# Kernel tuning notes

Hardware: AMD Instinct MI355X
Metric: run time of the kernel (lower is better)

The kernel has to match this reference:

```python
import jax, jax.numpy as jnp
import numpy as np

SEQ, D_IN, D_OUT = 8192, 768, 64


def setup_inputs() -> dict:
    key = jax.random.key(0)
    kx, kq, kk, kv = jax.random.split(key, 4)
    scale = 1.0 / np.sqrt(D_IN)
    return {
        "x": jax.random.normal(kx, (SEQ, D_IN), dtype=jnp.float32),
        # torch Linear weight layout: [d_out, d_in]
        "W_Q": jax.random.uniform(kq, (D_OUT, D_IN), dtype=jnp.float32, minval=-scale, maxval=scale),
        "W_K": jax.random.uniform(kk, (D_OUT, D_IN), dtype=jnp.float32, minval=-scale, maxval=scale),
        "W_V": jax.random.uniform(kv, (D_OUT, D_IN), dtype=jnp.float32, minval=-scale, maxval=scale),
    }


def reference(x, W_Q, W_K, W_V):
    # q,k,v: [seq, d_out]
    q = x @ W_Q.T
    k = x @ W_K.T
    v = x @ W_V.T
    scores = (q @ k.T) / jnp.sqrt(jnp.asarray(k.shape[-1], x.dtype))  # [seq, seq]
    attn = jax.nn.softmax(scores, axis=-1)
    return attn @ v  # [seq, d_out]
```

## Files before the change

kernel.cpp:

```cpp
#include <hip/hip_runtime.h>
#include <hip/hip_bf16.h>
#include <math.h>

#define SEQ 8192
#define DIN 768
#define DOUT 64
#define QSCALE 0.1803368801111214f

typedef __attribute__((ext_vector_type(8))) short short8;
typedef __attribute__((ext_vector_type(4))) short short4v;
typedef __attribute__((ext_vector_type(4))) float floatx4;
typedef __attribute__((ext_vector_type(2))) unsigned int uint2v;

__device__ __forceinline__ void gload16(const void* g, void* l) {
    __builtin_amdgcn_global_load_lds(
        (const __attribute__((address_space(1))) unsigned int*)g,
        (__attribute__((address_space(3))) unsigned int*)l, 16, 0, 0);
}

__device__ __forceinline__ unsigned pack2(float a, float b) {
    __hip_bfloat162 h = __float22bfloat162_rn(make_float2(a, b));
    return *(unsigned*)&h;
}

__device__ __forceinline__ unsigned short bfbits(float f) {
    __hip_bfloat16 h = __float2bfloat16(f);
    return *(unsigned short*)&h;
}

__device__ __forceinline__ float exp2r(float x) {
#if __has_builtin(__builtin_amdgcn_exp2f)
    return __builtin_amdgcn_exp2f(x);
#else
    float r; asm("v_exp_f32 %0, %1" : "=v"(r) : "v"(x)); return r;
#endif
}

__device__ __forceinline__ floatx4 max4(floatx4 a, floatx4 b) {
    floatx4 r;
    r[0] = fmaxf(a[0], b[0]); r[1] = fmaxf(a[1], b[1]);
    r[2] = fmaxf(a[2], b[2]); r[3] = fmaxf(a[3], b[3]);
    return r;
}

__device__ __forceinline__ floatx4 mfma16(short4v a, short4v b, floatx4 c) {
#if __has_builtin(__builtin_amdgcn_mfma_f32_16x16x16bf16_1k)
    return __builtin_amdgcn_mfma_f32_16x16x16bf16_1k(a, b, c, 0, 0, 0);
#else
    asm("v_mfma_f32_16x16x16_bf16 %0, %1, %2, %0" : "+v"(c) : "v"(a), "v"(b));
    return c;
#endif
}

__device__ __forceinline__ int phs(int s, int R) {
    return (s & 8) | ((s ^ R) & 7);
}

__global__ __launch_bounds__(256) void prep_w(
    const float* __restrict__ Wq, const float* __restrict__ Wk,
    const float* __restrict__ Wv, unsigned short* __restrict__ wbf)
{
    const int i = blockIdx.x * 256 + threadIdx.x;
    const int base = i * 8;
    const int row = base / DIN;
    const int k = base % DIN;
    const float* src = (row < 64)  ? &Wq[(size_t)row * DIN + k]
                     : (row < 128) ? &Wk[(size_t)(row - 64) * DIN + k]
                                   : &Wv[(size_t)(row - 128) * DIN + k];
    const float4 f0 = *(const float4*)src;
    const float4 f1 = *(const float4*)(src + 4);
    uint4 v;
    v.x = pack2(f0.x, f0.y);
    v.y = pack2(f0.z, f0.w);
    v.z = pack2(f1.x, f1.y);
    v.w = pack2(f1.z, f1.w);
    *(uint4*)&wbf[base] = v;
}

__global__ __launch_bounds__(256) void qkv_mfma(
    const float* __restrict__ x, const unsigned short* __restrict__ wbf,
    unsigned short* __restrict__ qbf, unsigned short* __restrict__ kbf,
    unsigned short* __restrict__ vtbf)
{
    __shared__ __align__(16) unsigned char xs[2][32 * 256];
    __shared__ __align__(16) unsigned char wsm[2][192 * 256];

    const int t = threadIdx.x;
    const int l = t & 63;
    const int wid = t >> 6;
    const int h = wid & 1;
    const int ntb = (wid >> 1) * 6;
    const int q4_ = l & 15;
    const int row0 = blockIdx.x * 32;

    const int Rx_st = t >> 3;
    const int s0    = (t & 7) * 2;
    const int Rr4   = l >> 4;
    const int s16   = l & 15;

    floatx4 acc[6];
#pragma unroll
    for (int i = 0; i < 6; ++i) acc[i] = (floatx4){0.f, 0.f, 0.f, 0.f};

#define STAGE_X(buf, k0)                                                      \
    {                                                                         \
        _Pragma("unroll")                                                     \
        for (int ss = 0; ss < 2; ++ss) {                                      \
            const int sl = s0 + ss;                                           \
            const float4 a = *(const float4*)&x[(size_t)(row0 + Rx_st) * DIN + (k0) + sl * 8]; \
            const float4 b = *(const float4*)&x[(size_t)(row0 + Rx_st) * DIN + (k0) + sl * 8 + 4]; \
            uint4 v;                                                          \
            v.x = pack2(a.x, a.y); v.y = pack2(a.z, a.w);                     \
            v.z = pack2(b.x, b.y); v.w = pack2(b.z, b.w);                     \
            *(uint4*)&xs[buf][Rx_st * 256 + phs(sl, Rx_st) * 16] = v;         \
        }                                                                     \
    }

#define STAGE_W(buf, k0)                                                      \
    {                                                                         \
        _Pragma("unroll")                                                     \
        for (int ss = 0; ss < 12; ++ss) {                                     \
            const int s = wid * 12 + ss;                           \
            const int Rw = 4 * s + Rr4;                           \
            const int slog = (s16 & 8) | ((s16 ^ Rw) & 7);                    \
            gload16(&wbf[(size_t)Rw * DIN + (k0) + slog * 8], &wsm[buf][s * 1024]); \
        }                                                                     \
    }

    STAGE_X(0, 0)
    STAGE_W(0, 0)

    int cur = 0;
    for (int kc = 0; kc < 6; ++kc) {
        __syncthreads();

        float4 xa[2], xb[2];
        const bool more = (kc + 1 < 6);
        if (more) {
            const int k1 = (kc + 1) * 128;
            STAGE_W(cur ^ 1, k1)
#pragma unroll
            for (int ss = 0; ss < 2; ++ss) {
                const int sl = s0 + ss;
                xa[ss] = *(const float4*)&x[(size_t)(row0 + Rx_st) * DIN + k1 + sl * 8];
                xb[ss] = *(const float4*)&x[(size_t)(row0 + Rx_st) * DIN + k1 + sl * 8 + 4];
            }
        }

#pragma unroll
        for (int ks = 0; ks < 4; ++ks) {
            const int g = l >> 4;
            const int slot = g + 4 * ks;
            const int Rxx = h * 16 + q4_;
            const short8 a = *(const short8*)&xs[cur][Rxx * 256 + phs(slot, Rxx) * 16];
#pragma unroll
            for (int j = 0; j < 6; ++j) {
                const int Rw = (ntb + j) * 16 + q4_;
                const short8 b = *(const short8*)&wsm[cur][Rw * 256 + phs(slot, Rw) * 16];
                acc[j] = __builtin_amdgcn_mfma_f32_16x16x32_bf16(a, b, acc[j], 0, 0, 0);
            }
        }

        if (more) {
#pragma unroll
            for (int ss = 0; ss < 2; ++ss) {
                const int sl = s0 + ss;
                uint4 v;
                v.x = pack2(xa[ss].x, xa[ss].y); v.y = pack2(xa[ss].z, xa[ss].w);
                v.z = pack2(xb[ss].x, xb[ss].y); v.w = pack2(xb[ss].z, xb[ss].w);
                *(uint4*)&xs[cur ^ 1][Rx_st * 256 + phs(sl, Rx_st) * 16] = v;
            }
        }
        cur ^= 1;
    }

    const int rb = row0 + h * 16 + ((l >> 4) << 2);
#pragma unroll
    for (int j = 0; j < 6; ++j) {
        const int nt = ntb + j;
#pragma unroll
        for (int r = 0; r < 4; ++r) {
            const float v = acc[j][r];
            const int R = rb + r;
            if (nt < 4) {
                qbf[(size_t)R * 64 + nt * 16 + q4_] = bfbits(v * QSCALE);
            } else if (nt < 8) {
                kbf[(size_t)R * 64 + (nt - 4) * 16 + q4_] = bfbits(v);
            } else {
                vtbf[(size_t)((nt - 8) * 16 + q4_) * SEQ + R] = bfbits(v);
            }
        }
    }
#undef STAGE_X
#undef STAGE_W
}

__global__ __launch_bounds__(256, 4) void flash_mfma(
    const unsigned short* __restrict__ qbf,
    const unsigned short* __restrict__ kbf,
    const unsigned short* __restrict__ vtbf,
    float* __restrict__ opart,
    float* __restrict__ ml,
    int nsplit, int direct)
{
    __shared__ __align__(16) unsigned char lds[32768];
    unsigned char* lkb = lds;
    unsigned char* lvb = lds + 16384;

    const int t = threadIdx.x;
    const int l = t & 63;
    const int g = l >> 4;
    const int q4 = l & 15;
    const int wid = t >> 6;
    const int row0 = blockIdx.x * 64;
    const int split = blockIdx.y;
    const int chunk = SEQ / nsplit;
    const int kbeg = split * chunk;
    const int NT = chunk / 64;

    short8 qf[2];
#pragma unroll
    for (int ks = 0; ks < 2; ++ks)
        qf[ks] = *(const short8*)&qbf[(size_t)(row0 + wid * 16 + q4) * 64 + (g + 4 * ks) * 8];

    {
        const int Rr = l >> 3;
        const int sl = (l & 7) ^ Rr;
#pragma unroll
        for (int ss = 0; ss < 2; ++ss) {
            const int s = wid * 2 + ss;
            const int R = 8 * s + Rr;
            gload16(&kbf[(size_t)(kbeg + R) * 64 + sl * 8], lkb + s * 1024);
            gload16(&vtbf[(size_t)R * SEQ + kbeg + sl * 8], lvb + s * 1024);
        }
    }
    __syncthreads();

    floatx4 oacc[4];
#pragma unroll
    for (int i = 0; i < 4; ++i) oacc[i] = (floatx4){0.f, 0.f, 0.f, 0.f};
    floatx4 l_acc = (floatx4){0.f, 0.f, 0.f, 0.f};
    float m_run = -INFINITY;

    int cur = 0;
    for (int tt = 0; tt < NT; ++tt) {
        const unsigned char* lk = lkb + cur * 8192;
        const unsigned char* lv = lvb + cur * 8192;

        if (tt + 1 < NT) {
            const int kt1 = kbeg + (tt + 1) * 64;
            const int Rr = l >> 3;
            const int sl = (l & 7) ^ Rr;
#pragma unroll
            for (int ss = 0; ss < 2; ++ss) {
                const int s = wid * 2 + ss;
                const int R = 8 * s + Rr;
                gload16(&kbf[(size_t)(kt1 + R) * 64 + sl * 8],
                        lkb + (cur ^ 1) * 8192 + s * 1024);
                gload16(&vtbf[(size_t)R * SEQ + kt1 + sl * 8],
                        lvb + (cur ^ 1) * 8192 + s * 1024);
            }
        }

        floatx4 sacc[4];
#pragma unroll
        for (int i = 0; i < 4; ++i) sacc[i] = (floatx4){0.f, 0.f, 0.f, 0.f};
#pragma unroll
        for (int ks = 0; ks < 2; ++ks) {
            const int sl = g + 4 * ks;
#pragma unroll
            for (int nt = 0; nt < 4; ++nt) {
                const int R = nt * 16 + q4;
                const short8 kf = *(const short8*)&lk[R * 128 + ((sl ^ (R & 7)) << 4)];
                sacc[nt] = __builtin_amdgcn_mfma_f32_16x16x32_bf16(kf, qf[ks], sacc[nt], 0, 0, 0);
            }
        }

        const floatx4 mm = max4(max4(sacc[0], sacc[1]), max4(sacc[2], sacc[3]));
        const float own = fmaxf(fmaxf(mm[0], mm[1]), fmaxf(mm[2], mm[3]));

        if (__any(own > m_run + 8.0f)) {
            float pm = own;
            pm = fmaxf(pm, __shfl_xor(pm, 16));
            pm = fmaxf(pm, __shfl_xor(pm, 32));
            const float mn = fmaxf(m_run, pm);
            const float alpha = exp2r(m_run - mn);
            m_run = mn;
            l_acc *= alpha;
#pragma unroll
            for (int dt = 0; dt < 4; ++dt) oacc[dt] *= alpha;
        }

        floatx4 pv4[4];
#pragma unroll
        for (int nt = 0; nt < 4; ++nt) {
            floatx4 d = sacc[nt];
            d[0] -= m_run; d[1] -= m_run; d[2] -= m_run; d[3] -= m_run;
            pv4[nt][0] = exp2r(d[0]); pv4[nt][1] = exp2r(d[1]);
            pv4[nt][2] = exp2r(d[2]); pv4[nt][3] = exp2r(d[3]);
        }
        l_acc += (pv4[0] + pv4[1]) + (pv4[2] + pv4[3]);

#pragma unroll
        for (int kb = 0; kb < 4; ++kb) {
            const unsigned p0 = pack2(pv4[kb][0], pv4[kb][1]);
            const unsigned p1 = pack2(pv4[kb][2], pv4[kb][3]);
            const short4v bfr = __builtin_bit_cast(short4v, (uint2v){p0, p1});
            const int sl = kb * 2 + (g >> 1);
#pragma unroll
            for (int dt = 0; dt < 4; ++dt) {
                const int R = dt * 16 + q4;
                const short4v a = *(const short4v*)&lv[R * 128 +
                    ((sl ^ (R & 7)) << 4) + ((g & 1) << 3)];
                oacc[dt] = mfma16(a, bfr, oacc[dt]);
            }
        }

        __syncthreads();
        cur ^= 1;
    }

    float l_run = (l_acc[0] + l_acc[1]) + (l_acc[2] + l_acc[3]);
    l_run += __shfl_xor(l_run, 16);
    l_run += __shfl_xor(l_run, 32);

    float* trans = (float*)lds;
    {
        const int qrow = wid * 16 + q4;
        const float sc = direct ? (1.0f / l_run) : 1.0f;
#pragma unroll
        for (int dt = 0; dt < 4; ++dt) {
            floatx4 v = oacc[dt] * sc;
            *(floatx4*)&trans[qrow * 68 + dt * 16 + g * 4] = v;
        }
        if (!direct && l < 16) {
            const size_t mrow = (size_t)split * SEQ + row0 + wid * 16 + l;
            ml[mrow * 2 + 0] = m_run;
            ml[mrow * 2 + 1] = l_run;
        }
    }
    __syncthreads();

    float* outbase = direct ? opart : opart + (size_t)split * SEQ * 64;
#pragma unroll
    for (int it = 0; it < 4; ++it) {
        const int row = it * 16 + (t >> 4);
        const floatx4 v = *(const floatx4*)&trans[row * 68 + (t & 15) * 4];
        *(floatx4*)&outbase[(size_t)(row0 + row) * 64 + (t & 15) * 4] = v;
    }
}

__global__ __launch_bounds__(256) void combine_kernel(
    const float* __restrict__ opart, const float* __restrict__ ml,
    float* __restrict__ out, int nsplit)
{
    const int i4 = blockIdx.x * 256 + threadIdx.x;
    if (i4 >= SEQ * DOUT / 4) return;
    const int row = (i4 * 4) >> 6;

    float M = -INFINITY;
    for (int s = 0; s < nsplit; ++s)
        M = fmaxf(M, ml[((size_t)s * SEQ + row) * 2]);

    float denom = 0.f;
    floatx4 acc = (floatx4){0.f, 0.f, 0.f, 0.f};
    for (int s = 0; s < nsplit; ++s) {
        const float w = exp2r(ml[((size_t)s * SEQ + row) * 2] - M);
        denom += ml[((size_t)s * SEQ + row) * 2 + 1] * w;
        const floatx4 v = *(const floatx4*)&opart[(size_t)s * SEQ * DOUT + i4 * 4];
        acc += v * w;
    }
    acc *= (1.0f / denom);
    *(floatx4*)&out[i4 * 4] = acc;
}

extern "C" void kernel_launch(void* const* d_in, const int* in_sizes, int n_in,
                              void* d_out, int out_size, void* d_ws, size_t ws_size,
                              hipStream_t stream)
{
    const float* x  = (const float*)d_in[0];
    const float* Wq = (const float*)d_in[1];
    const float* Wk = (const float*)d_in[2];
    const float* Wv = (const float*)d_in[3];
    float* out = (float*)d_out;
    unsigned char* ws = (unsigned char*)d_ws;

    const size_t wbf_b = (size_t)192 * DIN * 2;
    const size_t qkv_b = (size_t)SEQ * 64 * 2;
    size_t off = 0;
    unsigned short* wbf  = (unsigned short*)(ws + off); off += wbf_b;
    unsigned short* qbf  = (unsigned short*)(ws + off); off += qkv_b;
    unsigned short* kbf  = (unsigned short*)(ws + off); off += qkv_b;
    unsigned short* vtbf = (unsigned short*)(ws + off); off += qkv_b;

    const size_t per_split = (size_t)SEQ * 64 * 4 + (size_t)SEQ * 2 * 4;
    int nsplit = 0;
    if      (ws_size >= off + 8 * per_split) nsplit = 8;
    else if (ws_size >= off + 4 * per_split) nsplit = 4;
    else if (ws_size >= off + 2 * per_split) nsplit = 2;

    prep_w<<<72, 256, 0, stream>>>(Wq, Wk, Wv, wbf);
    qkv_mfma<<<SEQ / 32, 256, 0, stream>>>(x, wbf, qbf, kbf, vtbf);

    if (nsplit == 0) {
        flash_mfma<<<dim3(SEQ / 64, 1), 256, 0, stream>>>(
            qbf, kbf, vtbf, out, nullptr, 1, 1);
    } else {
        float* opart = (float*)(ws + off);
        float* mlp   = (float*)(ws + off + (size_t)nsplit * SEQ * 64 * 4);
        flash_mfma<<<dim3(SEQ / 64, nsplit), 256, 0, stream>>>(
            qbf, kbf, vtbf, opart, mlp, nsplit, 0);
        combine_kernel<<<(SEQ * DOUT / 4 + 255) / 256, 256, 0, stream>>>(
            opart, mlp, out, nsplit);
    }
}
```

Before: 61.22 us.

## Split key tiles across waves and load K/V straight into registers

The flash kernel is reorganized so each wave owns 16 keys of every 64-key tile for all 64 query rows, instead of owning 16 query rows. K and V fragments are loaded directly from global memory into registers with register prefetch. This removes the LDS double-buffering and the per-iteration block barrier. Partial outputs, maxima and sums from the four waves are merged through LDS at the end. In exchange the kernel needs many more accumulator registers (64 output floats per lane), drops the occupancy hint in launch bounds, and uses a running max shared across query tiles, which could hurt occupancy and numerical range.

```diff
diff --git a/kernel.cpp b/kernel.cpp
--- a/kernel.cpp
+++ b/kernel.cpp
@@ -120,8 +120,8 @@
     {                                                                         \
         _Pragma("unroll")                                                     \
         for (int ss = 0; ss < 12; ++ss) {                                     \
-            const int s = wid * 12 + ss;                           \
-            const int Rw = 4 * s + Rr4;                           \
+            const int s = wid * 12 + ss;                                      \
+            const int Rw = 4 * s + Rr4;                                       \
             const int slog = (s16 & 8) | ((s16 ^ Rw) & 7);                    \
             gload16(&wbf[(size_t)Rw * DIN + (k0) + slog * 8], &wsm[buf][s * 1024]); \
         }                                                                     \
@@ -195,7 +195,7 @@
 #undef STAGE_W
 }
 
-__global__ __launch_bounds__(256, 4) void flash_mfma(
+__global__ __launch_bounds__(256) void flash_mfma(
     const unsigned short* __restrict__ qbf,
     const unsigned short* __restrict__ kbf,
     const unsigned short* __restrict__ vtbf,
@@ -203,14 +203,14 @@
     float* __restrict__ ml,
     int nsplit, int direct)
 {
-    __shared__ __align__(16) unsigned char lds[32768];
-    unsigned char* lkb = lds;
-    unsigned char* lvb = lds + 16384;
+    __shared__ __align__(16) float obuf[2][64 * 68];
+    __shared__ float lbuf[4][64];
+    __shared__ float mbuf[4][16];
 
     const int t = threadIdx.x;
     const int l = t & 63;
+    const int x = l & 15;
     const int g = l >> 4;
-    const int q4 = l & 15;
     const int wid = t >> 6;
     const int row0 = blockIdx.x * 64;
     const int split = blockIdx.y;
@@ -218,62 +218,45 @@
     const int kbeg = split * chunk;
     const int NT = chunk / 64;
 
-    short8 qf[2];
-#pragma unroll
-    for (int ks = 0; ks < 2; ++ks)
-        qf[ks] = *(const short8*)&qbf[(size_t)(row0 + wid * 16 + q4) * 64 + (g + 4 * ks) * 8];
-
-    {
-        const int Rr = l >> 3;
-        const int sl = (l & 7) ^ Rr;
-#pragma unroll
-        for (int ss = 0; ss < 2; ++ss) {
-            const int s = wid * 2 + ss;
-            const int R = 8 * s + Rr;
-            gload16(&kbf[(size_t)(kbeg + R) * 64 + sl * 8], lkb + s * 1024);
-            gload16(&vtbf[(size_t)R * SEQ + kbeg + sl * 8], lvb + s * 1024);
-        }
-    }
-    __syncthreads();
-
-    floatx4 oacc[4];
-#pragma unroll
-    for (int i = 0; i < 4; ++i) oacc[i] = (floatx4){0.f, 0.f, 0.f, 0.f};
-    floatx4 l_acc = (floatx4){0.f, 0.f, 0.f, 0.f};
+    short8 qf[4][2];
+#pragma unroll
+    for (int qt = 0; qt < 4; ++qt)
+#pragma unroll
+        for (int ks = 0; ks < 2; ++ks)
+            qf[qt][ks] = *(const short8*)&qbf[(size_t)(row0 + qt * 16 + x) * 64 + ks * 32 + g * 8];
+
+    const unsigned short* kbase = kbf + (size_t)(kbeg + wid * 16 + x) * 64 + g * 8;
+    const unsigned short* vbase = vtbf + (size_t)x * SEQ + kbeg + wid * 16 + g * 4;
+
+    floatx4 oacc[4][4];
+#pragma unroll
+    for (int i = 0; i < 4; ++i)
+#pragma unroll
+        for (int j = 0; j < 4; ++j) oacc[i][j] = (floatx4){0.f, 0.f, 0.f, 0.f};
+    float l_acc[4] = {0.f, 0.f, 0.f, 0.f};
     float m_run = -INFINITY;
 
-    int cur = 0;
+    short8 kn0 = *(const short8*)(kbase);
+    short8 kn1 = *(const short8*)(kbase + 32);
+
     for (int tt = 0; tt < NT; ++tt) {
-        const unsigned char* lk = lkb + cur * 8192;
-        const unsigned char* lv = lvb + cur * 8192;
-
+        const short8 kc0 = kn0, kc1 = kn1;
         if (tt + 1 < NT) {
-            const int kt1 = kbeg + (tt + 1) * 64;
-            const int Rr = l >> 3;
-            const int sl = (l & 7) ^ Rr;
-#pragma unroll
-            for (int ss = 0; ss < 2; ++ss) {
-                const int s = wid * 2 + ss;
-                const int R = 8 * s + Rr;
-                gload16(&kbf[(size_t)(kt1 + R) * 64 + sl * 8],
-                        lkb + (cur ^ 1) * 8192 + s * 1024);
-                gload16(&vtbf[(size_t)R * SEQ + kt1 + sl * 8],
-                        lvb + (cur ^ 1) * 8192 + s * 1024);
-            }
-        }
+            kn0 = *(const short8*)(kbase + (size_t)(tt + 1) * 4096);
+            kn1 = *(const short8*)(kbase + (size_t)(tt + 1) * 4096 + 32);
+        }
+        short4v vf[4];
+#pragma unroll
+        for (int dt = 0; dt < 4; ++dt)
+            vf[dt] = *(const short4v*)(vbase + (size_t)dt * 16 * SEQ + tt * 64);
 
         floatx4 sacc[4];
 #pragma unroll
         for (int i = 0; i < 4; ++i) sacc[i] = (floatx4){0.f, 0.f, 0.f, 0.f};
 #pragma unroll
-        for (int ks = 0; ks < 2; ++ks) {
-            const int sl = g + 4 * ks;
-#pragma unroll
-            for (int nt = 0; nt < 4; ++nt) {
-                const int R = nt * 16 + q4;
-                const short8 kf = *(const short8*)&lk[R * 128 + ((sl ^ (R & 7)) << 4)];
-                sacc[nt] = __builtin_amdgcn_mfma_f32_16x16x32_bf16(kf, qf[ks], sacc[nt], 0, 0, 0);
-            }
+        for (int qt = 0; qt < 4; ++qt) {
+            sacc[qt] = __builtin_amdgcn_mfma_f32_16x16x32_bf16(kc0, qf[qt][0], sacc[qt], 0, 0, 0);
+            sacc[qt] = __builtin_amdgcn_mfma_f32_16x16x32_bf16(kc1, qf[qt][1], sacc[qt], 0, 0, 0);
         }
 
         const floatx4 mm = max4(max4(sacc[0], sacc[1]), max4(sacc[2], sacc[3]));
@@ -284,69 +267,103 @@
             pm = fmaxf(pm, __shfl_xor(pm, 16));
             pm = fmaxf(pm, __shfl_xor(pm, 32));
             const float mn = fmaxf(m_run, pm);
-            const float alpha = exp2r(m_run - mn);
+            const float al = exp2r(m_run - mn);
             m_run = mn;
-            l_acc *= alpha;
-#pragma unroll
-            for (int dt = 0; dt < 4; ++dt) oacc[dt] *= alpha;
-        }
-
-        floatx4 pv4[4];
-#pragma unroll
-        for (int nt = 0; nt < 4; ++nt) {
-            floatx4 d = sacc[nt];
+#pragma unroll
+            for (int qt = 0; qt < 4; ++qt) {
+                l_acc[qt] *= al;
+#pragma unroll
+                for (int dt = 0; dt < 4; ++dt) oacc[qt][dt] *= al;
+            }
+        }
+
+#pragma unroll
+        for (int qt = 0; qt < 4; ++qt) {
+            floatx4 d = sacc[qt];
             d[0] -= m_run; d[1] -= m_run; d[2] -= m_run; d[3] -= m_run;
-            pv4[nt][0] = exp2r(d[0]); pv4[nt][1] = exp2r(d[1]);
-            pv4[nt][2] = exp2r(d[2]); pv4[nt][3] = exp2r(d[3]);
-        }
-        l_acc += (pv4[0] + pv4[1]) + (pv4[2] + pv4[3]);
-
-#pragma unroll
-        for (int kb = 0; kb < 4; ++kb) {
-            const unsigned p0 = pack2(pv4[kb][0], pv4[kb][1]);
-            const unsigned p1 = pack2(pv4[kb][2], pv4[kb][3]);
-            const short4v bfr = __builtin_bit_cast(short4v, (uint2v){p0, p1});
-            const int sl = kb * 2 + (g >> 1);
+            floatx4 p;
+            p[0] = exp2r(d[0]); p[1] = exp2r(d[1]);
+            p[2] = exp2r(d[2]); p[3] = exp2r(d[3]);
+            l_acc[qt] += (p[0] + p[1]) + (p[2] + p[3]);
+            const unsigned p0 = pack2(p[0], p[1]);
+            const unsigned p1 = pack2(p[2], p[3]);
+            const short4v pb = __builtin_bit_cast(short4v, (uint2v){p0, p1});
+#pragma unroll
+            for (int dt = 0; dt < 4; ++dt)
+                oacc[qt][dt] = mfma16(vf[dt], pb, oacc[qt][dt]);
+        }
+    }
+
+    if (l < 16) mbuf[wid][x] = m_run;
+    __syncthreads();
+
+    const float Mx = fmaxf(fmaxf(mbuf[0][x], mbuf[1][x]),
+                           fmaxf(mbuf[2][x], mbuf[3][x]));
+    const float scale = exp2r(m_run - Mx);
+
+    float lq[4];
+#pragma unroll
+    for (int qt = 0; qt < 4; ++qt) {
+        float s = l_acc[qt];
+        s += __shfl_xor(s, 16);
+        s += __shfl_xor(s, 32);
+        lq[qt] = s * scale;
+    }
+    if (l < 16) {
+#pragma unroll
+        for (int qt = 0; qt < 4; ++qt) lbuf[wid][qt * 16 + x] = lq[qt];
+    }
+
+    float* mybuf = obuf[wid >> 1];
+    if (wid & 1) {
+#pragma unroll
+        for (int qt = 0; qt < 4; ++qt)
+#pragma unroll
+            for (int dt = 0; dt < 4; ++dt)
+                *(floatx4*)&mybuf[(qt * 16 + x) * 68 + dt * 16 + g * 4] =
+                    oacc[qt][dt] * scale;
+    }
+    __syncthreads();
+    if (!(wid & 1)) {
+#pragma unroll
+        for (int qt = 0; qt < 4; ++qt)
 #pragma unroll
             for (int dt = 0; dt < 4; ++dt) {
-                const int R = dt * 16 + q4;
-                const short4v a = *(const short4v*)&lv[R * 128 +
-                    ((sl ^ (R & 7)) << 4) + ((g & 1) << 3)];
-                oacc[dt] = mfma16(a, bfr, oacc[dt]);
-            }
-        }
-
-        __syncthreads();
-        cur ^= 1;
-    }
-
-    float l_run = (l_acc[0] + l_acc[1]) + (l_acc[2] + l_acc[3]);
-    l_run += __shfl_xor(l_run, 16);
-    l_run += __shfl_xor(l_run, 32);
-
-    float* trans = (float*)lds;
-    {
-        const int qrow = wid * 16 + q4;
-        const float sc = direct ? (1.0f / l_run) : 1.0f;
-#pragma unroll
-        for (int dt = 0; dt < 4; ++dt) {
-            floatx4 v = oacc[dt] * sc;
-            *(floatx4*)&trans[qrow * 68 + dt * 16 + g * 4] = v;
-        }
-        if (!direct && l < 16) {
-            const size_t mrow = (size_t)split * SEQ + row0 + wid * 16 + l;
-            ml[mrow * 2 + 0] = m_run;
-            ml[mrow * 2 + 1] = l_run;
-        }
+                const int idx = (qt * 16 + x) * 68 + dt * 16 + g * 4;
+                floatx4 v = *(const floatx4*)&mybuf[idx];
+                v += oacc[qt][dt] * scale;
+                *(floatx4*)&mybuf[idx] = v;
+            }
     }
     __syncthreads();
 
-    float* outbase = direct ? opart : opart + (size_t)split * SEQ * 64;
-#pragma unroll
-    for (int it = 0; it < 4; ++it) {
-        const int row = it * 16 + (t >> 4);
-        const floatx4 v = *(const floatx4*)&trans[row * 68 + (t & 15) * 4];
-        *(floatx4*)&outbase[(size_t)(row0 + row) * 64 + (t & 15) * 4] = v;
+    const int q = t >> 2;
+    const int c = t & 3;
+    const float lrow = lbuf[0][q] + lbuf[1][q] + lbuf[2][q] + lbuf[3][q];
+
+    if (direct) {
+        const float inv = 1.0f / lrow;
+#pragma unroll
+        for (int j = 0; j < 4; ++j) {
+            const int idx = q * 68 + c * 16 + 4 * j;
+            floatx4 v = *(const floatx4*)&obuf[0][idx] + *(const floatx4*)&obuf[1][idx];
+            *(floatx4*)&opart[(size_t)(row0 + q) * 64 + c * 16 + 4 * j] = v * inv;
+        }
+    } else {
+        float* outp = opart + (size_t)split * SEQ * 64;
+#pragma unroll
+        for (int j = 0; j < 4; ++j) {
+            const int idx = q * 68 + c * 16 + 4 * j;
+            floatx4 v = *(const floatx4*)&obuf[0][idx] + *(const floatx4*)&obuf[1][idx];
+            *(floatx4*)&outp[(size_t)(row0 + q) * 64 + c * 16 + 4 * j] = v;
+        }
+        if (c == 0) {
+            const float Mq = fmaxf(fmaxf(mbuf[0][q & 15], mbuf[1][q & 15]),
+                                   fmaxf(mbuf[2][q & 15], mbuf[3][q & 15]));
+            const size_t mrow = (size_t)split * SEQ + row0 + q;
+            ml[mrow * 2 + 0] = Mq;
+            ml[mrow * 2 + 1] = lrow;
+        }
     }
 }
 
```

Result: slower. 85.42 us (+39.5%).

## Retile QKV projection to 64-row blocks with 64-wide K chunks; add MFMA setprio

Applied to the files above, without the earlier changes.

The QKV projection kernel now uses 512-thread blocks covering 64 rows instead of 32. Each projected weight tile is therefore reused across twice as many rows, and the grid is halved. K is staged in 64-wide chunks over 12 iterations instead of 128-wide over 6, which uses a simpler XOR swizzle and less LDS per buffer. s_setprio hints are also wrapped around the MFMA sections in both the projection and flash kernels, to favour matrix issue over other waves. The cost is more loop iterations and barriers, and fewer blocks to fill the GPU.

```diff
diff --git a/kernel.cpp b/kernel.cpp
--- a/kernel.cpp
+++ b/kernel.cpp
@@ -50,10 +50,6 @@
     asm("v_mfma_f32_16x16x16_bf16 %0, %1, %2, %0" : "+v"(c) : "v"(a), "v"(b));
     return c;
 #endif
-}
-
-__device__ __forceinline__ int phs(int s, int R) {
-    return (s & 8) | ((s ^ R) & 7);
 }
 
 __global__ __launch_bounds__(256) void prep_w(
@@ -77,26 +73,27 @@
     *(uint4*)&wbf[base] = v;
 }
 
-__global__ __launch_bounds__(256) void qkv_mfma(
+__global__ __launch_bounds__(512) void qkv_mfma(
     const float* __restrict__ x, const unsigned short* __restrict__ wbf,
     unsigned short* __restrict__ qbf, unsigned short* __restrict__ kbf,
     unsigned short* __restrict__ vtbf)
 {
-    __shared__ __align__(16) unsigned char xs[2][32 * 256];
-    __shared__ __align__(16) unsigned char wsm[2][192 * 256];
+    __shared__ __align__(16) unsigned char xs[2][64 * 128];
+    __shared__ __align__(16) unsigned char wsm[2][192 * 128];
 
     const int t = threadIdx.x;
     const int l = t & 63;
     const int wid = t >> 6;
-    const int h = wid & 1;
-    const int ntb = (wid >> 1) * 6;
-    const int q4_ = l & 15;
-    const int row0 = blockIdx.x * 32;
+    const int h = wid & 3;
+    const int ntb = (wid >> 2) * 6;
+    const int g = l >> 4;
+    const int q4 = l & 15;
+    const int row0 = blockIdx.x * 64;
 
     const int Rx_st = t >> 3;
-    const int s0    = (t & 7) * 2;
-    const int Rr4   = l >> 4;
-    const int s16   = l & 15;
+    const int slx   = t & 7;
+    const int Rr    = l >> 3;
+    const int sld   = (l & 7) ^ Rr;
 
     floatx4 acc[6];
 #pragma unroll
@@ -104,26 +101,21 @@
 
 #define STAGE_X(buf, k0)                                                      \
     {                                                                         \
-        _Pragma("unroll")                                                     \
-        for (int ss = 0; ss < 2; ++ss) {                                      \
-            const int sl = s0 + ss;                                           \
-            const float4 a = *(const float4*)&x[(size_t)(row0 + Rx_st) * DIN + (k0) + sl * 8]; \
-            const float4 b = *(const float4*)&x[(size_t)(row0 + Rx_st) * DIN + (k0) + sl * 8 + 4]; \
-            uint4 v;                                                          \
-            v.x = pack2(a.x, a.y); v.y = pack2(a.z, a.w);                     \
-            v.z = pack2(b.x, b.y); v.w = pack2(b.z, b.w);                     \
-            *(uint4*)&xs[buf][Rx_st * 256 + phs(sl, Rx_st) * 16] = v;         \
-        }                                                                     \
+        const float4 a = *(const float4*)&x[(size_t)(row0 + Rx_st) * DIN + (k0) + slx * 8]; \
+        const float4 b = *(const float4*)&x[(size_t)(row0 + Rx_st) * DIN + (k0) + slx * 8 + 4]; \
+        uint4 v;                                                              \
+        v.x = pack2(a.x, a.y); v.y = pack2(a.z, a.w);                         \
+        v.z = pack2(b.x, b.y); v.w = pack2(b.z, b.w);                         \
+        *(uint4*)&xs[buf][Rx_st * 128 + ((slx ^ (Rx_st & 7)) << 4)] = v;      \
     }
 
 #define STAGE_W(buf, k0)                                                      \
     {                                                                         \
         _Pragma("unroll")                                                     \
-        for (int ss = 0; ss < 12; ++ss) {                                     \
-            const int s = wid * 12 + ss;                           \
-            const int Rw = 4 * s + Rr4;                           \
-            const int slog = (s16 & 8) | ((s16 ^ Rw) & 7);                    \
-            gload16(&wbf[(size_t)Rw * DIN + (k0) + slog * 8], &wsm[buf][s * 1024]); \
+        for (int ss = 0; ss < 3; ++ss) {                                      \
+            const int s = wid * 3 + ss;                            \
+            const int Rw = 8 * s + Rr;                            \
+            gload16(&wbf[(size_t)Rw * DIN + (k0) + sld * 8], &wsm[buf][s * 1024]); \
         }                                                                     \
     }
 
@@ -131,50 +123,43 @@
     STAGE_W(0, 0)
 
     int cur = 0;
-    for (int kc = 0; kc < 6; ++kc) {
+    for (int kc = 0; kc < 12; ++kc) {
         __syncthreads();
 
-        float4 xa[2], xb[2];
-        const bool more = (kc + 1 < 6);
+        float4 xa, xb;
+        const bool more = (kc + 1 < 12);
         if (more) {
-            const int k1 = (kc + 1) * 128;
+            const int k1 = (kc + 1) * 64;
             STAGE_W(cur ^ 1, k1)
-#pragma unroll
-            for (int ss = 0; ss < 2; ++ss) {
-                const int sl = s0 + ss;
-                xa[ss] = *(const float4*)&x[(size_t)(row0 + Rx_st) * DIN + k1 + sl * 8];
-                xb[ss] = *(const float4*)&x[(size_t)(row0 + Rx_st) * DIN + k1 + sl * 8 + 4];
-            }
-        }
-
-#pragma unroll
-        for (int ks = 0; ks < 4; ++ks) {
-            const int g = l >> 4;
-            const int slot = g + 4 * ks;
-            const int Rxx = h * 16 + q4_;
-            const short8 a = *(const short8*)&xs[cur][Rxx * 256 + phs(slot, Rxx) * 16];
+            xa = *(const float4*)&x[(size_t)(row0 + Rx_st) * DIN + k1 + slx * 8];
+            xb = *(const float4*)&x[(size_t)(row0 + Rx_st) * DIN + k1 + slx * 8 + 4];
+        }
+
+        __builtin_amdgcn_s_setprio(1);
+#pragma unroll
+        for (int ks = 0; ks < 2; ++ks) {
+            const int sl = g + 4 * ks;
+            const int Rx = h * 16 + q4;
+            const short8 a = *(const short8*)&xs[cur][Rx * 128 + ((sl ^ (Rx & 7)) << 4)];
 #pragma unroll
             for (int j = 0; j < 6; ++j) {
-                const int Rw = (ntb + j) * 16 + q4_;
-                const short8 b = *(const short8*)&wsm[cur][Rw * 256 + phs(slot, Rw) * 16];
+                const int Rw = (ntb + j) * 16 + q4;
+                const short8 b = *(const short8*)&wsm[cur][Rw * 128 + ((sl ^ (Rw & 7)) << 4)];
                 acc[j] = __builtin_amdgcn_mfma_f32_16x16x32_bf16(a, b, acc[j], 0, 0, 0);
             }
         }
+        __builtin_amdgcn_s_setprio(0);
 
         if (more) {
-#pragma unroll
-            for (int ss = 0; ss < 2; ++ss) {
-                const int sl = s0 + ss;
-                uint4 v;
-                v.x = pack2(xa[ss].x, xa[ss].y); v.y = pack2(xa[ss].z, xa[ss].w);
-                v.z = pack2(xb[ss].x, xb[ss].y); v.w = pack2(xb[ss].z, xb[ss].w);
-                *(uint4*)&xs[cur ^ 1][Rx_st * 256 + phs(sl, Rx_st) * 16] = v;
-            }
+            uint4 v;
+            v.x = pack2(xa.x, xa.y); v.y = pack2(xa.z, xa.w);
+            v.z = pack2(xb.x, xb.y); v.w = pack2(xb.z, xb.w);
+            *(uint4*)&xs[cur ^ 1][Rx_st * 128 + ((slx ^ (Rx_st & 7)) << 4)] = v;
         }
         cur ^= 1;
     }
 
-    const int rb = row0 + h * 16 + ((l >> 4) << 2);
+    const int rb = row0 + h * 16 + (g << 2);
 #pragma unroll
     for (int j = 0; j < 6; ++j) {
         const int nt = ntb + j;
@@ -183,11 +168,11 @@
             const float v = acc[j][r];
             const int R = rb + r;
             if (nt < 4) {
-                qbf[(size_t)R * 64 + nt * 16 + q4_] = bfbits(v * QSCALE);
+                qbf[(size_t)R * 64 + nt * 16 + q4] = bfbits(v * QSCALE);
             } else if (nt < 8) {
-                kbf[(size_t)R * 64 + (nt - 4) * 16 + q4_] = bfbits(v);
+                kbf[(size_t)R * 64 + (nt - 4) * 16 + q4] = bfbits(v);
             } else {
-                vtbf[(size_t)((nt - 8) * 16 + q4_) * SEQ + R] = bfbits(v);
+                vtbf[(size_t)((nt - 8) * 16 + q4) * SEQ + R] = bfbits(v);
             }
         }
     }
@@ -265,6 +250,7 @@
         floatx4 sacc[4];
 #pragma unroll
         for (int i = 0; i < 4; ++i) sacc[i] = (floatx4){0.f, 0.f, 0.f, 0.f};
+        __builtin_amdgcn_s_setprio(1);
 #pragma unroll
         for (int ks = 0; ks < 2; ++ks) {
             const int sl = g + 4 * ks;
@@ -275,6 +261,7 @@
                 sacc[nt] = __builtin_amdgcn_mfma_f32_16x16x32_bf16(kf, qf[ks], sacc[nt], 0, 0, 0);
             }
         }
+        __builtin_amdgcn_s_setprio(0);
 
         const floatx4 mm = max4(max4(sacc[0], sacc[1]), max4(sacc[2], sacc[3]));
         const float own = fmaxf(fmaxf(mm[0], mm[1]), fmaxf(mm[2], mm[3]));
@@ -301,6 +288,7 @@
         }
         l_acc += (pv4[0] + pv4[1]) + (pv4[2] + pv4[3]);
 
+        __builtin_amdgcn_s_setprio(1);
 #pragma unroll
         for (int kb = 0; kb < 4; ++kb) {
             const unsigned p0 = pack2(pv4[kb][0], pv4[kb][1]);
@@ -315,6 +303,7 @@
                 oacc[dt] = mfma16(a, bfr, oacc[dt]);
             }
         }
+        __builtin_amdgcn_s_setprio(0);
 
         __syncthreads();
         cur ^= 1;
@@ -400,7 +389,7 @@
     else if (ws_size >= off + 2 * per_split) nsplit = 2;
 
     prep_w<<<72, 256, 0, stream>>>(Wq, Wk, Wv, wbf);
-    qkv_mfma<<<SEQ / 32, 256, 0, stream>>>(x, wbf, qbf, kbf, vtbf);
+    qkv_mfma<<<SEQ / 64, 512, 0, stream>>>(x, wbf, qbf, kbf, vtbf);
 
     if (nsplit == 0) {
         flash_mfma<<<dim3(SEQ / 64, 1), 256, 0, stream>>>(
```

After: 64.15 us. 4.8% more time.
